# Optimization experiments

Hardware: AMD Instinct MI355X
Metric: run time of the kernel (lower is better)

Reference implementation:

```python
import jax, jax.numpy as jnp
import numpy as np

D = 256
N = 131072


def setup_inputs() -> dict:
    key = jax.random.key(0)
    kx, ku = jax.random.split(key)
    X = jax.random.normal(kx, (N, D), dtype=jnp.float32)
    U = jax.random.normal(ku, (D, D), dtype=jnp.float32) * 0.5
    # reset_parameters: normalize each row of U
    U = U / jnp.linalg.norm(U, axis=1, keepdims=True)
    return {"X": X, "U": U}


def reference(X, U):
    # sequential_mult iterates rows from d-1 down to 0, so scan over flipped U.
    def step(Xc, v):
        # v: [d];  X <- X - 2 * (X v) v^T / (v.v)
        coef = (Xc @ v) * (2.0 / jnp.dot(v, v))  # [N]
        Xc = Xc - coef[:, None] * v[None, :]
        return Xc, None

    Xout, _ = jax.lax.scan(step, X, U[::-1])
    return Xout
```

## Files before the change

### kernel.cpp

```cpp
#include <hip/hip_runtime.h>
#include <hip/hip_bf16.h>

typedef __attribute__((ext_vector_type(8))) short short8;
typedef __attribute__((ext_vector_type(4))) float f32x4;

#define DDIM 256
#define NROWS 131072
#define ROWS_PER_BLK 128
#define GBLK ((NROWS / ROWS_PER_BLK) * 2)

static __device__ __forceinline__ unsigned short f2bf(float f){
  unsigned b = __builtin_bit_cast(unsigned, f);
  b += 0x7FFFu + ((b >> 16) & 1u);
  return (unsigned short)(b >> 16);
}

static __device__ __forceinline__ float wave_sum_bcast(float x){
  int v = __builtin_bit_cast(int, x);
#define DPP_ADD(ctrl)                                                          \
  v = __builtin_bit_cast(int,                                                  \
        __builtin_bit_cast(float, v) +                                         \
        __builtin_bit_cast(float,                                              \
          __builtin_amdgcn_update_dpp(0, v, (ctrl), 0xF, 0xF, true)))
  DPP_ADD(0x111);
  DPP_ADD(0x112);
  DPP_ADD(0x114);
  DPP_ADD(0x118);
  DPP_ADD(0x142);
  DPP_ADD(0x143);
#undef DPP_ADD
  return __builtin_bit_cast(float, __builtin_amdgcn_readlane(v, 63));
}

__global__ __launch_bounds__(256) void compute_beta(const float* __restrict__ U,
                                                    float* __restrict__ beta){
  const int lane = threadIdx.x & 63;
  const int k = blockIdx.x * 4 + (threadIdx.x >> 6);
  const f32x4 a = *reinterpret_cast<const f32x4*>(U + (size_t)k * 256 + lane * 4);
  const float s = wave_sum_bcast(a[0]*a[0] + a[1]*a[1] + a[2]*a[2] + a[3]*a[3]);
  if (lane == 0) beta[k] = 2.0f / s;
}

__global__ __launch_bounds__(256) void compute_q(const float* __restrict__ U,
                                                 const float* __restrict__ beta,
                                                 unsigned short* __restrict__ Qt){
  const int lane = threadIdx.x & 63;
  const int wv   = threadIdx.x >> 6;
  const int pair = blockIdx.x * 4 + wv;
  const int j0 = pair * 2, j1 = j0 + 1;

  float u0[4], u1[4], r0[4], r1[4], r2[4], r3[4];
#pragma unroll
  for (int e = 0; e < 4; ++e){
    const int i = e * 64 + lane;
    u0[e] = (i == j0) ? 1.f : 0.f;
    u1[e] = (i == j1) ? 1.f : 0.f;
    r0[e] = U[0 * 256 + i];
    r1[e] = U[1 * 256 + i];
    r2[e] = U[2 * 256 + i];
    r3[e] = U[3 * 256 + i];
  }
  float b0 = beta[0], b1 = beta[1], b2 = beta[2], b3 = beta[3];

#define QSTEP(R, B, KN)                                                        \
  do {                                                                         \
    const float p0_ = (u0[0]*R[0] + u0[1]*R[1]) + (u0[2]*R[2] + u0[3]*R[3]);   \
    const float p1_ = (u1[0]*R[0] + u1[1]*R[1]) + (u1[2]*R[2] + u1[3]*R[3]);   \
    const float d0_ = wave_sum_bcast(p0_);                                     \
    const float d1_ = wave_sum_bcast(p1_);                                     \
    const float c0_ = d0_ * B, c1_ = d1_ * B;                                  \
    _Pragma("unroll")                                                          \
    for (int e = 0; e < 4; ++e){                                               \
      u0[e] = fmaf(-c0_, R[e], u0[e]);                                         \
      u1[e] = fmaf(-c1_, R[e], u1[e]);                                         \
      R[e] = U[(size_t)(KN) * 256 + e * 64 + lane];                            \
    }                                                                          \
    B = beta[(KN)];                                                            \
  } while (0)

  for (int k = 0; k < 256; k += 4){
    const int k4 = (k+4) & 255, k5 = (k+5) & 255, k6 = (k+6) & 255, k7 = (k+7) & 255;
    QSTEP(r0, b0, k4);
    QSTEP(r1, b1, k5);
    QSTEP(r2, b2, k6);
    QSTEP(r3, b3, k7);
  }
#undef QSTEP

#pragma unroll
  for (int e = 0; e < 4; ++e){
    const int i = e * 64 + lane;
    Qt[(size_t)j0 * 256 + i] = f2bf(u0[e]);
    Qt[(size_t)j1 * 256 + i] = f2bf(u1[e]);
  }
}

__global__ __launch_bounds__(512, 4) void gemm_xq(const float* __restrict__ X,
                                                  const unsigned short* __restrict__ Qt,
                                                  float* __restrict__ Y){
  __shared__ char qb[65536];

  const int tid  = threadIdx.x;
  const int lane = tid & 63;
  const int wv   = tid >> 6;
  const int lg   = lane >> 4;
  const int lm   = lane & 15;
  const int half = blockIdx.x & 1;
  const size_t rg = blockIdx.x >> 1;
  const size_t row0 = rg * ROWS_PER_BLK + wv * 16;

  f32x4 sv[8];
#pragma unroll
  for (int it = 0; it < 8; ++it){
    const int c = tid + it * 512;
    sv[it] = *reinterpret_cast<const f32x4*>(
        reinterpret_cast<const char*>(Qt) +
        ((size_t)(half * 128) << 9) + ((size_t)c << 4));
  }

  const float* xp = X + (row0 + lm) * DDIM + lg * 8;
  f32x4 xv[16];
#pragma unroll
  for (int kk = 0; kk < 8; ++kk){
    xv[2*kk]   = *reinterpret_cast<const f32x4*>(xp + kk * 32);
    xv[2*kk+1] = *reinterpret_cast<const f32x4*>(xp + kk * 32 + 4);
  }

#pragma unroll
  for (int it = 0; it < 8; ++it){
    const int c   = tid + it * 512;
    const int n   = c >> 5;
    const int off = (c & 31) << 4;
    *reinterpret_cast<f32x4*>(qb + (n << 9) + (off ^ ((n & 15) << 5))) = sv[it];
  }
  __syncthreads();

  f32x4 acc[8];
#pragma unroll
  for (int nt = 0; nt < 8; ++nt) acc[nt] = (f32x4){0.f, 0.f, 0.f, 0.f};

#pragma unroll
  for (int kk = 0; kk < 8; ++kk){
    const f32x4 lo = xv[2*kk], hi = xv[2*kk+1];
    short8 a;
    a[0] = (short)f2bf(lo[0]); a[1] = (short)f2bf(lo[1]);
    a[2] = (short)f2bf(lo[2]); a[3] = (short)f2bf(lo[3]);
    a[4] = (short)f2bf(hi[0]); a[5] = (short)f2bf(hi[1]);
    a[6] = (short)f2bf(hi[2]); a[7] = (short)f2bf(hi[3]);

    const int kb = kk * 64 + (lg << 4);
#pragma unroll
    for (int nt = 0; nt < 8; ++nt){
      const int nl = nt * 16 + lm;
      const short8 b = *reinterpret_cast<const short8*>(
          qb + (nl << 9) + (kb ^ ((nl & 15) << 5)));
      acc[nt] = __builtin_amdgcn_mfma_f32_16x16x32_bf16(a, b, acc[nt], 0, 0, 0);
    }
  }

  const size_t orow = row0 + lg * 4;
  const int col0 = half * 128;
#pragma unroll
  for (int nt = 0; nt < 8; ++nt){
#pragma unroll
    for (int r = 0; r < 4; ++r){
      Y[(orow + r) * DDIM + col0 + nt * 16 + lm] = acc[nt][r];
    }
  }
}

extern "C" void kernel_launch(void* const* d_in, const int* in_sizes, int n_in,
                              void* d_out, int out_size, void* d_ws, size_t ws_size,
                              hipStream_t stream) {
  const float* X = (const float*)d_in[0];
  const float* U = (const float*)d_in[1];
  float* Y = (float*)d_out;
  unsigned short* Qt = (unsigned short*)d_ws;

  float* beta = (float*)d_out + ((size_t)out_size - 256);

  compute_beta<<<64, 256, 0, stream>>>(U, beta);
  compute_q<<<32, 256, 0, stream>>>(U, beta, Qt);
  gemm_xq<<<GBLK, 512, 0, stream>>>(X, Qt, Y);
}
```

Baseline: 110.9 us.

## Make GEMM blocks persistent over row chunks with a prefetch ring; fold beta into compute_q

The GEMM grid shrinks to 512 blocks, and each block loops over four 128-row chunks. X fragments are prefetched four steps ahead in a register ring, so one block keeps the Q tile in LDS and overlaps X loads with MFMA work. The separate compute_beta launch is removed: each step of compute_q now computes v·v with an extra wave reduction and a fast reciprocal. This saves one kernel launch but adds reduction work and lowers precision in the serial Q build.

New measurement: 120.0 us. +8.1%, slower.

```diff
diff --git a/kernel.cpp b/kernel.cpp
--- a/kernel.cpp
+++ b/kernel.cpp
@@ -6,8 +6,11 @@
 
 #define DDIM 256
 #define NROWS 131072
-#define ROWS_PER_BLK 128
-#define GBLK ((NROWS / ROWS_PER_BLK) * 2)
+#define RG 256
+#define GBLK (RG * 2)
+#define RPG (NROWS / RG)
+#define CHUNK 128
+#define NSTEP 32
 
 static __device__ __forceinline__ unsigned short f2bf(float f){
   unsigned b = __builtin_bit_cast(unsigned, f);
@@ -32,17 +35,7 @@
   return __builtin_bit_cast(float, __builtin_amdgcn_readlane(v, 63));
 }
 
-__global__ __launch_bounds__(256) void compute_beta(const float* __restrict__ U,
-                                                    float* __restrict__ beta){
-  const int lane = threadIdx.x & 63;
-  const int k = blockIdx.x * 4 + (threadIdx.x >> 6);
-  const f32x4 a = *reinterpret_cast<const f32x4*>(U + (size_t)k * 256 + lane * 4);
-  const float s = wave_sum_bcast(a[0]*a[0] + a[1]*a[1] + a[2]*a[2] + a[3]*a[3]);
-  if (lane == 0) beta[k] = 2.0f / s;
-}
-
 __global__ __launch_bounds__(256) void compute_q(const float* __restrict__ U,
-                                                 const float* __restrict__ beta,
                                                  unsigned short* __restrict__ Qt){
   const int lane = threadIdx.x & 63;
   const int wv   = threadIdx.x >> 6;
@@ -60,30 +53,31 @@
     r2[e] = U[2 * 256 + i];
     r3[e] = U[3 * 256 + i];
   }
-  float b0 = beta[0], b1 = beta[1], b2 = beta[2], b3 = beta[3];
 
-#define QSTEP(R, B, KN)                                                        \
+#define QSTEP(R, KN)                                                           \
   do {                                                                         \
     const float p0_ = (u0[0]*R[0] + u0[1]*R[1]) + (u0[2]*R[2] + u0[3]*R[3]);   \
     const float p1_ = (u1[0]*R[0] + u1[1]*R[1]) + (u1[2]*R[2] + u1[3]*R[3]);   \
+    const float pv_ = (R[0]*R[0] + R[1]*R[1]) + (R[2]*R[2] + R[3]*R[3]);       \
     const float d0_ = wave_sum_bcast(p0_);                                     \
     const float d1_ = wave_sum_bcast(p1_);                                     \
-    const float c0_ = d0_ * B, c1_ = d1_ * B;                                  \
+    const float dv_ = wave_sum_bcast(pv_);                                     \
+    const float inv_ = 2.0f * __builtin_amdgcn_rcpf(dv_);                      \
+    const float c0_ = d0_ * inv_, c1_ = d1_ * inv_;                            \
     _Pragma("unroll")                                                          \
     for (int e = 0; e < 4; ++e){                                               \
       u0[e] = fmaf(-c0_, R[e], u0[e]);                                         \
       u1[e] = fmaf(-c1_, R[e], u1[e]);                                         \
       R[e] = U[(size_t)(KN) * 256 + e * 64 + lane];                            \
     }                                                                          \
-    B = beta[(KN)];                                                            \
   } while (0)
 
   for (int k = 0; k < 256; k += 4){
     const int k4 = (k+4) & 255, k5 = (k+5) & 255, k6 = (k+6) & 255, k7 = (k+7) & 255;
-    QSTEP(r0, b0, k4);
-    QSTEP(r1, b1, k5);
-    QSTEP(r2, b2, k6);
-    QSTEP(r3, b3, k7);
+    QSTEP(r0, k4);
+    QSTEP(r1, k5);
+    QSTEP(r2, k6);
+    QSTEP(r3, k7);
   }
 #undef QSTEP
 
@@ -107,7 +101,7 @@
   const int lm   = lane & 15;
   const int half = blockIdx.x & 1;
   const size_t rg = blockIdx.x >> 1;
-  const size_t row0 = rg * ROWS_PER_BLK + wv * 16;
+  const size_t rowbase = rg * RPG;
 
   f32x4 sv[8];
 #pragma unroll
@@ -118,13 +112,17 @@
         ((size_t)(half * 128) << 9) + ((size_t)c << 4));
   }
 
-  const float* xp = X + (row0 + lm) * DDIM + lg * 8;
-  f32x4 xv[16];
-#pragma unroll
-  for (int kk = 0; kk < 8; ++kk){
-    xv[2*kk]   = *reinterpret_cast<const f32x4*>(xp + kk * 32);
-    xv[2*kk+1] = *reinterpret_cast<const f32x4*>(xp + kk * 32 + 4);
-  }
+  const float* xl = X + (rowbase + wv * 16 + lm) * DDIM + lg * 8;
+
+  f32x4 f[4][2];
+#define LDX(slot, s)                                                           \
+  do {                                                                         \
+    const float* p_ = xl + (size_t)((s) >> 3) * (CHUNK * DDIM) + ((s) & 7) * 32;\
+    f[slot][0] = *reinterpret_cast<const f32x4*>(p_);                          \
+    f[slot][1] = *reinterpret_cast<const f32x4*>(p_ + 4);                      \
+  } while (0)
+
+  LDX(0, 0); LDX(1, 1); LDX(2, 2); LDX(3, 3);
 
 #pragma unroll
   for (int it = 0; it < 8; ++it){
@@ -140,33 +138,38 @@
   for (int nt = 0; nt < 8; ++nt) acc[nt] = (f32x4){0.f, 0.f, 0.f, 0.f};
 
 #pragma unroll
-  for (int kk = 0; kk < 8; ++kk){
-    const f32x4 lo = xv[2*kk], hi = xv[2*kk+1];
-    short8 a;
-    a[0] = (short)f2bf(lo[0]); a[1] = (short)f2bf(lo[1]);
-    a[2] = (short)f2bf(lo[2]); a[3] = (short)f2bf(lo[3]);
-    a[4] = (short)f2bf(hi[0]); a[5] = (short)f2bf(hi[1]);
-    a[6] = (short)f2bf(hi[2]); a[7] = (short)f2bf(hi[3]);
-
-    const int kb = kk * 64 + (lg << 4);
+  for (int s = 0; s < NSTEP; ++s){
+    {
+      const f32x4 lo = f[s & 3][0], hi = f[s & 3][1];
+      short8 a;
+      a[0] = (short)f2bf(lo[0]); a[1] = (short)f2bf(lo[1]);
+      a[2] = (short)f2bf(lo[2]); a[3] = (short)f2bf(lo[3]);
+      a[4] = (short)f2bf(hi[0]); a[5] = (short)f2bf(hi[1]);
+      a[6] = (short)f2bf(hi[2]); a[7] = (short)f2bf(hi[3]);
+      const int kb = (s & 7) * 64 + (lg << 4);
 #pragma unroll
-    for (int nt = 0; nt < 8; ++nt){
-      const int nl = nt * 16 + lm;
-      const short8 b = *reinterpret_cast<const short8*>(
-          qb + (nl << 9) + (kb ^ ((nl & 15) << 5)));
-      acc[nt] = __builtin_amdgcn_mfma_f32_16x16x32_bf16(a, b, acc[nt], 0, 0, 0);
+      for (int nt = 0; nt < 8; ++nt){
+        const int nl = nt * 16 + lm;
+        const short8 b = *reinterpret_cast<const short8*>(
+            qb + (nl << 9) + (kb ^ ((nl & 15) << 5)));
+        acc[nt] = __builtin_amdgcn_mfma_f32_16x16x32_bf16(a, b, acc[nt], 0, 0, 0);
+      }
+    }
+    if (s + 4 < NSTEP) LDX(s & 3, s + 4);
+    if ((s & 7) == 7){
+      const int c = s >> 3;
+      const size_t orow = rowbase + (size_t)c * CHUNK + wv * 16 + lg * 4;
+#pragma unroll
+      for (int nt = 0; nt < 8; ++nt){
+#pragma unroll
+        for (int r = 0; r < 4; ++r){
+          Y[(orow + r) * DDIM + half * 128 + nt * 16 + lm] = acc[nt][r];
+        }
+        acc[nt] = (f32x4){0.f, 0.f, 0.f, 0.f};
+      }
     }
   }
-
-  const size_t orow = row0 + lg * 4;
-  const int col0 = half * 128;
-#pragma unroll
-  for (int nt = 0; nt < 8; ++nt){
-#pragma unroll
-    for (int r = 0; r < 4; ++r){
-      Y[(orow + r) * DDIM + col0 + nt * 16 + lm] = acc[nt][r];
-    }
-  }
+#undef LDX
 }
 
 extern "C" void kernel_launch(void* const* d_in, const int* in_sizes, int n_in,
@@ -177,9 +180,6 @@
   float* Y = (float*)d_out;
   unsigned short* Qt = (unsigned short*)d_ws;
 
-  float* beta = (float*)d_out + ((size_t)out_size - 256);
-
-  compute_beta<<<64, 256, 0, stream>>>(U, beta);
-  compute_q<<<32, 256, 0, stream>>>(U, beta, Qt);
+  compute_q<<<32, 256, 0, stream>>>(U, Qt);
   gemm_xq<<<GBLK, 512, 0, stream>>>(X, Qt, Y);
 }
```
